# Optimization experiments

Hardware: AMD Instinct MI355X
Metric: run time of the kernel (lower is better)

The kernel has to match this reference:

```python
import jax, jax.numpy as jnp
import numpy as np

FP16_HUGE = 65504.0  # large additive mask constant (fp16-max style, as in AF2 torch ports)

B, N, T = 1, 384, 4
CQ, CT = 128, 64      # query (pair) channels, template pair channels
H = 4                 # num heads
D = CT // H           # per-head key/value dim = 16 (AF2: key_dim=value_dim=64 split over 4 heads)


def setup_inputs() -> dict:
    key = jax.random.key(0)
    ks = jax.random.split(key, 8)
    inp = {
        "query_embedding": jax.random.normal(ks[0], (B, N, N, CQ), jnp.float32),
        "template_pair_representation": jax.random.normal(ks[1], (B, T, N, N, CT), jnp.float32),
        "template_mask": jnp.ones((B, T), jnp.float32),
        # attention params (gating=False for template pointwise attention in AF2)
        "query_w": jax.random.normal(ks[2], (H, CQ, D), jnp.float32) * (CQ ** -0.5),
        "key_w": jax.random.normal(ks[3], (H, CT, D), jnp.float32) * (CT ** -0.5),
        "value_w": jax.random.normal(ks[4], (H, CT, D), jnp.float32) * (CT ** -0.5),
        "output_w": jax.random.normal(ks[5], (H, D, CQ), jnp.float32) * ((H * D) ** -0.5),
        "output_b": jnp.zeros((CQ,), jnp.float32),
    }
    return inp


def reference(query_embedding, template_pair_representation, template_mask,
              query_w, key_w, value_w, output_w, output_b):
    b, n, _, cq = query_embedding.shape
    t = template_mask.shape[-1]
    d = query_w.shape[-1]

    # [b, n*n, 1, cq]: each (i,j) pair position attends over templates
    flat_q = query_embedding.reshape(b, n * n, 1, cq)
    # [b, t, n, n, ct] -> [b, n, n, t, ct] -> [b, n*n, t, ct]
    flat_t = jnp.transpose(template_pair_representation, (0, 2, 3, 1, 4)).reshape(b, n * n, t, -1)

    # additive bias over key axis: 0 where mask=1, -FP16_HUGE where mask=0; [b,1,1,1,t]
    bias = FP16_HUGE * (template_mask[:, None, None, None, :] - 1.0)

    q = jnp.einsum('bpic,hcd->bphid', flat_q, query_w) * (d ** -0.5)  # [b,p,h,1,d]
    k = jnp.einsum('bptc,hcd->bphtd', flat_t, key_w)                  # [b,p,h,t,d]
    v = jnp.einsum('bptc,hcd->bphtd', flat_t, value_w)

    logits = jnp.einsum('bphid,bphtd->bphit', q, k) + bias            # [b,p,h,1,t]
    weights = jax.nn.softmax(logits, axis=-1)
    wv = jnp.einsum('bphit,bphtd->bphid', weights, v)                 # [b,p,h,1,d]
    out = jnp.einsum('bphid,hdc->bpic', wv, output_w) + output_b      # [b,p,1,cq]

    embedding = out.reshape(b, n, n, cq)
    tmask = (jnp.sum(template_mask.reshape(b, -1), axis=1) > 0.0).astype(embedding.dtype)
    return embedding * tmask[:, None, None, None]
```

## Files before the change

### kernel.cpp

```cpp
#include <hip/hip_runtime.h>
#include <hip/hip_bf16.h>

typedef __attribute__((ext_vector_type(8))) short bf16x8;
typedef __attribute__((ext_vector_type(4))) float f32x4;

#define NPOS 147456
#define NTILES 9216
#define TPW 2
#define WPB 4
#define NBLK (NTILES / (TPW * WPB))

__device__ inline short bfc(float f) {
  union { __hip_bfloat16 h; short s; } u;
  u.h = __float2bfloat16(f);
  return u.s;
}

__global__ __launch_bounds__(256, 2) void tpa_kernel(
    const float* __restrict__ qe, const float* __restrict__ tpr,
    const float* __restrict__ tmk_p, const float* __restrict__ wq,
    const float* __restrict__ wk, const float* __restrict__ wv,
    const float* __restrict__ wo, const float* __restrict__ ob,
    float* __restrict__ out)
{
  __shared__ unsigned short wqT[8192];
  __shared__ unsigned short woT[8192];
  __shared__ unsigned short wvbuf[WPB][1024];

  const int tid   = threadIdx.x;
  const int wid   = tid >> 6;
  const int lane  = tid & 63;
  const int row16 = lane & 15;
  const int grp   = lane >> 4;

  for (int e = tid; e < 8192; e += 256) {
    {
      int h = e >> 11, c = (e >> 4) & 127, d = e & 15;
      int col = h * 16 + d;
      wqT[(col * 128 + c) ^ ((col & 7) << 3)] = (unsigned short)bfc(wq[e] * 0.25f);
    }
    {
      int h = e >> 11, d = (e >> 7) & 15, cq = e & 127;
      int k = h * 16 + d;
      woT[(cq * 64 + k) ^ ((cq & 7) << 3)] = (unsigned short)bfc(wo[e]);
    }
  }

  bf16x8 bk[4][2], bv[4][2];
  #pragma unroll
  for (int n = 0; n < 4; ++n)
    #pragma unroll
    for (int kc = 0; kc < 2; ++kc)
      #pragma unroll
      for (int e = 0; e < 8; ++e) {
        int c = kc * 32 + grp * 8 + e;
        bk[n][kc][e] = bfc(wk[n * 1024 + c * 16 + row16]);
        bv[n][kc][e] = bfc(wv[n * 1024 + c * 16 + row16]);
      }

  const float m0 = tmk_p[0], m1 = tmk_p[1], m2 = tmk_p[2], m3 = tmk_p[3];
  const float biasv[4] = {65504.0f * (m0 - 1.0f), 65504.0f * (m1 - 1.0f),
                          65504.0f * (m2 - 1.0f), 65504.0f * (m3 - 1.0f)};
  const float tmk = (m0 + m1 + m2 + m3 > 0.0f) ? 1.0f : 0.0f;

  float obr[8];
  #pragma unroll
  for (int n8 = 0; n8 < 8; ++n8) obr[n8] = ob[n8 * 16 + row16] * tmk;

  __syncthreads();

  const int gwave = blockIdx.x * WPB + wid;

  for (int it = 0; it < TPW; ++it) {
    const int p0 = (gwave * TPW + it) * 16;

    f32x4 qv[8];
    {
      const f32x4* qbase = reinterpret_cast<const f32x4*>(qe) + (p0 + row16) * 32 + grp * 2;
      #pragma unroll
      for (int kc = 0; kc < 4; ++kc) {
        qv[kc * 2 + 0] = qbase[kc * 8 + 0];
        qv[kc * 2 + 1] = qbase[kc * 8 + 1];
      }
    }
    f32x4 tv[4][4];
    #pragma unroll
    for (int t = 0; t < 4; ++t) {
      const f32x4* tbase = reinterpret_cast<const f32x4*>(tpr) + (t * NPOS + p0 + row16) * 16 + grp * 2;
      #pragma unroll
      for (int kc = 0; kc < 2; ++kc) {
        tv[t][kc * 2 + 0] = tbase[kc * 8 + 0];
        tv[t][kc * 2 + 1] = tbase[kc * 8 + 1];
      }
    }

    bf16x8 aq[4];
    #pragma unroll
    for (int kc = 0; kc < 4; ++kc)
      #pragma unroll
      for (int e = 0; e < 8; ++e)
        aq[kc][e] = bfc(e < 4 ? qv[kc * 2 + 0][e] : qv[kc * 2 + 1][e - 4]);

    f32x4 qT[4];
    #pragma unroll
    for (int n = 0; n < 4; ++n) {
      qT[n] = (f32x4){0.f, 0.f, 0.f, 0.f};
      #pragma unroll
      for (int kc = 0; kc < 4; ++kc) {
        const bf16x8 a = *reinterpret_cast<const bf16x8*>(
            &wqT[(((n * 16 + row16) * 128) + kc * 32 + grp * 8) ^ ((row16 & 7) << 3)]);
        qT[n] = __builtin_amdgcn_mfma_f32_16x16x32_bf16(a, aq[kc], qT[n], 0, 0, 0);
      }
    }

    float ssum[4] = {0.f, 0.f, 0.f, 0.f};
    f32x4 wvT[4];
    #pragma unroll
    for (int n = 0; n < 4; ++n) wvT[n] = (f32x4){0.f, 0.f, 0.f, 0.f};

    #pragma unroll
    for (int t = 0; t < 4; ++t) {
      bf16x8 at[2];
      #pragma unroll
      for (int kc = 0; kc < 2; ++kc)
        #pragma unroll
        for (int e = 0; e < 8; ++e)
          at[kc][e] = bfc(e < 4 ? tv[t][kc * 2 + 0][e] : tv[t][kc * 2 + 1][e - 4]);

      f32x4 kT[4], vT[4];
      #pragma unroll
      for (int n = 0; n < 4; ++n) {
        kT[n] = (f32x4){0.f, 0.f, 0.f, 0.f};
        vT[n] = (f32x4){0.f, 0.f, 0.f, 0.f};
        #pragma unroll
        for (int kc = 0; kc < 2; ++kc) {
          kT[n] = __builtin_amdgcn_mfma_f32_16x16x32_bf16(bk[n][kc], at[kc], kT[n], 0, 0, 0);
          vT[n] = __builtin_amdgcn_mfma_f32_16x16x32_bf16(bv[n][kc], at[kc], vT[n], 0, 0, 0);
        }
      }
      #pragma unroll
      for (int n = 0; n < 4; ++n) {
        float lg = qT[n][0] * kT[n][0] + qT[n][1] * kT[n][1] +
                   qT[n][2] * kT[n][2] + qT[n][3] * kT[n][3];
        lg += __shfl_xor(lg, 16);
        lg += __shfl_xor(lg, 32);
        const float w = __expf(lg + biasv[t]);
        ssum[n] += w;
        #pragma unroll
        for (int r = 0; r < 4; ++r) wvT[n][r] += w * vT[n][r];
      }
    }

    #pragma unroll
    for (int n = 0; n < 4; ++n) {
      const float inv = tmk / fmaxf(ssum[n], 1e-30f);
      #pragma unroll
      for (int r = 0; r < 4; ++r) {
        const int hd = n * 16 + grp * 4 + r;
        wvbuf[wid][(row16 * 64 + hd) ^ ((row16 & 7) << 3)] =
            (unsigned short)bfc(wvT[n][r] * inv);
      }
    }
    asm volatile("s_waitcnt lgkmcnt(0)" ::: "memory");
    __builtin_amdgcn_sched_barrier(0);

    bf16x8 awv[2];
    #pragma unroll
    for (int kc = 0; kc < 2; ++kc)
      awv[kc] = *reinterpret_cast<const bf16x8*>(
          &wvbuf[wid][(row16 * 64 + kc * 32 + grp * 8) ^ ((row16 & 7) << 3)]);

    const int orow0 = p0 + grp * 4;
    #pragma unroll
    for (int n8 = 0; n8 < 8; ++n8) {
      f32x4 acc = (f32x4){0.f, 0.f, 0.f, 0.f};
      #pragma unroll
      for (int kc = 0; kc < 2; ++kc) {
        const bf16x8 b = *reinterpret_cast<const bf16x8*>(
            &woT[(((n8 * 16 + row16) * 64) + kc * 32 + grp * 8) ^ ((row16 & 7) << 3)]);
        acc = __builtin_amdgcn_mfma_f32_16x16x32_bf16(awv[kc], b, acc, 0, 0, 0);
      }
      #pragma unroll
      for (int r = 0; r < 4; ++r)
        out[(orow0 + r) * 128 + n8 * 16 + row16] = acc[r] + obr[n8];
    }
  }
}

extern "C" void kernel_launch(void* const* d_in, const int* in_sizes, int n_in,
                              void* d_out, int out_size, void* d_ws, size_t ws_size,
                              hipStream_t stream) {
  const float* qe  = (const float*)d_in[0];
  const float* tpr = (const float*)d_in[1];
  const float* tmk = (const float*)d_in[2];
  const float* wq  = (const float*)d_in[3];
  const float* wk  = (const float*)d_in[4];
  const float* wv  = (const float*)d_in[5];
  const float* wo  = (const float*)d_in[6];
  const float* ob  = (const float*)d_in[7];
  float* out = (float*)d_out;

  tpa_kernel<<<NBLK, 256, 0, stream>>>(qe, tpr, tmk, wq, wk, wv, wo, ob, out);
}
```

Before: 76.14 us.

## Pre-swizzle weights into MFMA fragments and use one-wave blocks per tile

```diff
diff --git a/kernel.cpp b/kernel.cpp
--- a/kernel.cpp
+++ b/kernel.cpp
@@ -3,187 +3,175 @@
 
 typedef __attribute__((ext_vector_type(8))) short bf16x8;
 typedef __attribute__((ext_vector_type(4))) float f32x4;
+typedef unsigned int u32;
+typedef unsigned short u16;
 
 #define NPOS 147456
 #define NTILES 9216
-#define TPW 2
-#define WPB 4
-#define NBLK (NTILES / (TPW * WPB))
 
-__device__ inline short bfc(float f) {
-  union { __hip_bfloat16 h; short s; } u;
+__device__ inline u16 bfc(float f) {
+  union { __hip_bfloat16 h; u16 s; } u;
   u.h = __float2bfloat16(f);
   return u.s;
 }
 
-__global__ __launch_bounds__(256, 2) void tpa_kernel(
+__global__ void prep_kernel(const float* __restrict__ wq, const float* __restrict__ wk,
+                            const float* __restrict__ wv, const float* __restrict__ wo,
+                            u16* __restrict__ wsf) {
+  int gid = blockIdx.x * 256 + threadIdx.x;
+  int idx, which;
+  if (gid < 8192)       { idx = gid;         which = 0; }
+  else if (gid < 12288) { idx = gid - 8192;  which = 1; }
+  else if (gid < 16384) { idx = gid - 12288; which = 2; }
+  else                  { idx = gid - 16384; which = 3; }
+  int fragid = idx >> 9, lane = (idx >> 3) & 63, e = idx & 7;
+  int l15 = lane & 15, g = lane >> 4;
+  float v;
+  if (which == 0) {
+    int n = fragid >> 2, kc = fragid & 3;
+    int c = kc * 32 + g * 8 + e;
+    v = wq[n * 2048 + c * 16 + l15] * 0.25f;
+  } else if (which == 1) {
+    int n = fragid >> 1, kc = fragid & 1;
+    int c = kc * 32 + g * 8 + e;
+    v = wk[n * 1024 + c * 16 + l15];
+  } else if (which == 2) {
+    int n = fragid >> 1, kc = fragid & 1;
+    int c = kc * 32 + g * 8 + e;
+    v = wv[n * 1024 + c * 16 + l15];
+  } else {
+    int n8 = fragid >> 1, kc = fragid & 1;
+    int hd = kc * 32 + g * 8 + e;
+    v = wo[(hd >> 4) * 2048 + (hd & 15) * 128 + n8 * 16 + l15];
+  }
+  wsf[gid] = bfc(v);
+}
+
+#define WQF(n, kc)  ((      (n) * 4 + (kc)) * 64)
+#define WKF(n, kc)  (1024 + ((n) * 2 + (kc)) * 64)
+#define WVF(n, kc)  (1536 + ((n) * 2 + (kc)) * 64)
+#define WOF(n8, kc) (2048 + ((n8) * 2 + (kc)) * 64)
+
+__global__ __launch_bounds__(64, 4) void tpa_kernel(
     const float* __restrict__ qe, const float* __restrict__ tpr,
-    const float* __restrict__ tmk_p, const float* __restrict__ wq,
-    const float* __restrict__ wk, const float* __restrict__ wv,
-    const float* __restrict__ wo, const float* __restrict__ ob,
-    float* __restrict__ out)
+    const float* __restrict__ tmk_p, const float* __restrict__ ob,
+    const u16* __restrict__ wsf, float* __restrict__ out)
 {
-  __shared__ unsigned short wqT[8192];
-  __shared__ unsigned short woT[8192];
-  __shared__ unsigned short wvbuf[WPB][1024];
-
-  const int tid   = threadIdx.x;
-  const int wid   = tid >> 6;
-  const int lane  = tid & 63;
-  const int row16 = lane & 15;
-  const int grp   = lane >> 4;
-
-  for (int e = tid; e < 8192; e += 256) {
-    {
-      int h = e >> 11, c = (e >> 4) & 127, d = e & 15;
-      int col = h * 16 + d;
-      wqT[(col * 128 + c) ^ ((col & 7) << 3)] = (unsigned short)bfc(wq[e] * 0.25f);
-    }
-    {
-      int h = e >> 11, d = (e >> 7) & 15, cq = e & 127;
-      int k = h * 16 + d;
-      woT[(cq * 64 + k) ^ ((cq & 7) << 3)] = (unsigned short)bfc(wo[e]);
-    }
-  }
-
-  bf16x8 bk[4][2], bv[4][2];
-  #pragma unroll
-  for (int n = 0; n < 4; ++n)
-    #pragma unroll
-    for (int kc = 0; kc < 2; ++kc)
-      #pragma unroll
-      for (int e = 0; e < 8; ++e) {
-        int c = kc * 32 + grp * 8 + e;
-        bk[n][kc][e] = bfc(wk[n * 1024 + c * 16 + row16]);
-        bv[n][kc][e] = bfc(wv[n * 1024 + c * 16 + row16]);
-      }
+  const int lane = threadIdx.x;
+  const int l15 = lane & 15, g = lane >> 4;
+  const int p0 = blockIdx.x * 16;
+  const bf16x8* __restrict__ wf = reinterpret_cast<const bf16x8*>(wsf);
 
   const float m0 = tmk_p[0], m1 = tmk_p[1], m2 = tmk_p[2], m3 = tmk_p[3];
   const float biasv[4] = {65504.0f * (m0 - 1.0f), 65504.0f * (m1 - 1.0f),
                           65504.0f * (m2 - 1.0f), 65504.0f * (m3 - 1.0f)};
   const float tmk = (m0 + m1 + m2 + m3 > 0.0f) ? 1.0f : 0.0f;
 
-  float obr[8];
+  const f32x4* qbase = reinterpret_cast<const f32x4*>(qe) + (p0 + l15) * 32 + g * 2;
+  f32x4 qv[8];
   #pragma unroll
-  for (int n8 = 0; n8 < 8; ++n8) obr[n8] = ob[n8 * 16 + row16] * tmk;
+  for (int kc = 0; kc < 4; ++kc) {
+    qv[kc * 2 + 0] = qbase[kc * 8 + 0];
+    qv[kc * 2 + 1] = qbase[kc * 8 + 1];
+  }
+  f32x4 tv[4][4];
+  #pragma unroll
+  for (int t = 0; t < 2; ++t) {
+    const f32x4* tbase = reinterpret_cast<const f32x4*>(tpr) +
+                         ((size_t)t * NPOS + p0 + l15) * 16 + g * 2;
+    #pragma unroll
+    for (int kc = 0; kc < 2; ++kc) {
+      tv[t][kc * 2 + 0] = tbase[kc * 8 + 0];
+      tv[t][kc * 2 + 1] = tbase[kc * 8 + 1];
+    }
+  }
 
-  __syncthreads();
+  f32x4 qT[4];
+  #pragma unroll
+  for (int n = 0; n < 4; ++n) qT[n] = (f32x4){0.f, 0.f, 0.f, 0.f};
+  #pragma unroll
+  for (int kc = 0; kc < 4; ++kc) {
+    bf16x8 aq;
+    #pragma unroll
+    for (int e = 0; e < 8; ++e)
+      aq[e] = (short)bfc(e < 4 ? qv[kc * 2 + 0][e] : qv[kc * 2 + 1][e - 4]);
+    #pragma unroll
+    for (int n = 0; n < 4; ++n)
+      qT[n] = __builtin_amdgcn_mfma_f32_16x16x32_bf16(wf[WQF(n, kc) + lane], aq, qT[n], 0, 0, 0);
+  }
 
-  const int gwave = blockIdx.x * WPB + wid;
+  float ssum[4] = {0.f, 0.f, 0.f, 0.f};
+  f32x4 wvT[4];
+  #pragma unroll
+  for (int n = 0; n < 4; ++n) wvT[n] = (f32x4){0.f, 0.f, 0.f, 0.f};
 
-  for (int it = 0; it < TPW; ++it) {
-    const int p0 = (gwave * TPW + it) * 16;
-
-    f32x4 qv[8];
-    {
-      const f32x4* qbase = reinterpret_cast<const f32x4*>(qe) + (p0 + row16) * 32 + grp * 2;
+  #pragma unroll
+  for (int t = 0; t < 4; ++t) {
+    if (t < 2) {
+      const f32x4* tbase = reinterpret_cast<const f32x4*>(tpr) +
+                           ((size_t)(t + 2) * NPOS + p0 + l15) * 16 + g * 2;
       #pragma unroll
-      for (int kc = 0; kc < 4; ++kc) {
-        qv[kc * 2 + 0] = qbase[kc * 8 + 0];
-        qv[kc * 2 + 1] = qbase[kc * 8 + 1];
+      for (int kc = 0; kc < 2; ++kc) {
+        tv[t + 2][kc * 2 + 0] = tbase[kc * 8 + 0];
+        tv[t + 2][kc * 2 + 1] = tbase[kc * 8 + 1];
       }
     }
-    f32x4 tv[4][4];
+    bf16x8 at0, at1;
     #pragma unroll
-    for (int t = 0; t < 4; ++t) {
-      const f32x4* tbase = reinterpret_cast<const f32x4*>(tpr) + (t * NPOS + p0 + row16) * 16 + grp * 2;
+    for (int e = 0; e < 8; ++e) {
+      at0[e] = (short)bfc(e < 4 ? tv[t][0][e] : tv[t][1][e - 4]);
+      at1[e] = (short)bfc(e < 4 ? tv[t][2][e] : tv[t][3][e - 4]);
+    }
+    #pragma unroll
+    for (int n = 0; n < 4; ++n) {
+      f32x4 kT = (f32x4){0.f, 0.f, 0.f, 0.f};
+      f32x4 vT = (f32x4){0.f, 0.f, 0.f, 0.f};
+      kT = __builtin_amdgcn_mfma_f32_16x16x32_bf16(wf[WKF(n, 0) + lane], at0, kT, 0, 0, 0);
+      kT = __builtin_amdgcn_mfma_f32_16x16x32_bf16(wf[WKF(n, 1) + lane], at1, kT, 0, 0, 0);
+      vT = __builtin_amdgcn_mfma_f32_16x16x32_bf16(wf[WVF(n, 0) + lane], at0, vT, 0, 0, 0);
+      vT = __builtin_amdgcn_mfma_f32_16x16x32_bf16(wf[WVF(n, 1) + lane], at1, vT, 0, 0, 0);
+      float lg = qT[n][0] * kT[0] + qT[n][1] * kT[1] + qT[n][2] * kT[2] + qT[n][3] * kT[3];
+      lg += __shfl_xor(lg, 16);
+      lg += __shfl_xor(lg, 32);
+      const float w = __expf(lg + biasv[t]);
+      ssum[n] += w;
       #pragma unroll
-      for (int kc = 0; kc < 2; ++kc) {
-        tv[t][kc * 2 + 0] = tbase[kc * 8 + 0];
-        tv[t][kc * 2 + 1] = tbase[kc * 8 + 1];
-      }
+      for (int r = 0; r < 4; ++r) wvT[n][r] += w * vT[r];
+    }
+  }
+
+  u32 pk[4][2];
+  #pragma unroll
+  for (int n = 0; n < 4; ++n) {
+    const float inv = tmk / fmaxf(ssum[n], 1e-30f);
+    pk[n][0] = (u32)bfc(wvT[n][0] * inv) | ((u32)bfc(wvT[n][1] * inv) << 16);
+    pk[n][1] = (u32)bfc(wvT[n][2] * inv) | ((u32)bfc(wvT[n][3] * inv) << 16);
+  }
+
+  union { u32 w[4]; bf16x8 v; } awv[2];
+  #pragma unroll
+  for (int kc = 0; kc < 2; ++kc)
+    #pragma unroll
+    for (int w = 0; w < 4; ++w) {
+      const int j = w & 1, hi = w >> 1;
+      const int src = l15 + 16 * ((g & 1) * 2 + hi);
+      const u32 t0 = __shfl(pk[kc * 2 + 0][j], src);
+      const u32 t1 = __shfl(pk[kc * 2 + 1][j], src);
+      awv[kc].w[w] = (g >> 1) ? t1 : t0;
     }
 
-    bf16x8 aq[4];
+  const f32x4* obase = reinterpret_cast<const f32x4*>(ob);
+  f32x4* orow = reinterpret_cast<f32x4*>(out + (size_t)(p0 + l15) * 128);
+  #pragma unroll
+  for (int n8 = 0; n8 < 8; ++n8) {
+    f32x4 acc = (f32x4){0.f, 0.f, 0.f, 0.f};
+    acc = __builtin_amdgcn_mfma_f32_16x16x32_bf16(wf[WOF(n8, 0) + lane], awv[0].v, acc, 0, 0, 0);
+    acc = __builtin_amdgcn_mfma_f32_16x16x32_bf16(wf[WOF(n8, 1) + lane], awv[1].v, acc, 0, 0, 0);
+    const f32x4 obf = obase[n8 * 4 + g];
+    f32x4 res;
     #pragma unroll
-    for (int kc = 0; kc < 4; ++kc)
-      #pragma unroll
-      for (int e = 0; e < 8; ++e)
-        aq[kc][e] = bfc(e < 4 ? qv[kc * 2 + 0][e] : qv[kc * 2 + 1][e - 4]);
-
-    f32x4 qT[4];
-    #pragma unroll
-    for (int n = 0; n < 4; ++n) {
-      qT[n] = (f32x4){0.f, 0.f, 0.f, 0.f};
-      #pragma unroll
-      for (int kc = 0; kc < 4; ++kc) {
-        const bf16x8 a = *reinterpret_cast<const bf16x8*>(
-            &wqT[(((n * 16 + row16) * 128) + kc * 32 + grp * 8) ^ ((row16 & 7) << 3)]);
-        qT[n] = __builtin_amdgcn_mfma_f32_16x16x32_bf16(a, aq[kc], qT[n], 0, 0, 0);
-      }
-    }
-
-    float ssum[4] = {0.f, 0.f, 0.f, 0.f};
-    f32x4 wvT[4];
-    #pragma unroll
-    for (int n = 0; n < 4; ++n) wvT[n] = (f32x4){0.f, 0.f, 0.f, 0.f};
-
-    #pragma unroll
-    for (int t = 0; t < 4; ++t) {
-      bf16x8 at[2];
-      #pragma unroll
-      for (int kc = 0; kc < 2; ++kc)
-        #pragma unroll
-        for (int e = 0; e < 8; ++e)
-          at[kc][e] = bfc(e < 4 ? tv[t][kc * 2 + 0][e] : tv[t][kc * 2 + 1][e - 4]);
-
-      f32x4 kT[4], vT[4];
-      #pragma unroll
-      for (int n = 0; n < 4; ++n) {
-        kT[n] = (f32x4){0.f, 0.f, 0.f, 0.f};
-        vT[n] = (f32x4){0.f, 0.f, 0.f, 0.f};
-        #pragma unroll
-        for (int kc = 0; kc < 2; ++kc) {
-          kT[n] = __builtin_amdgcn_mfma_f32_16x16x32_bf16(bk[n][kc], at[kc], kT[n], 0, 0, 0);
-          vT[n] = __builtin_amdgcn_mfma_f32_16x16x32_bf16(bv[n][kc], at[kc], vT[n], 0, 0, 0);
-        }
-      }
-      #pragma unroll
-      for (int n = 0; n < 4; ++n) {
-        float lg = qT[n][0] * kT[n][0] + qT[n][1] * kT[n][1] +
-                   qT[n][2] * kT[n][2] + qT[n][3] * kT[n][3];
-        lg += __shfl_xor(lg, 16);
-        lg += __shfl_xor(lg, 32);
-        const float w = __expf(lg + biasv[t]);
-        ssum[n] += w;
-        #pragma unroll
-        for (int r = 0; r < 4; ++r) wvT[n][r] += w * vT[n][r];
-      }
-    }
-
-    #pragma unroll
-    for (int n = 0; n < 4; ++n) {
-      const float inv = tmk / fmaxf(ssum[n], 1e-30f);
-      #pragma unroll
-      for (int r = 0; r < 4; ++r) {
-        const int hd = n * 16 + grp * 4 + r;
-        wvbuf[wid][(row16 * 64 + hd) ^ ((row16 & 7) << 3)] =
-            (unsigned short)bfc(wvT[n][r] * inv);
-      }
-    }
-    asm volatile("s_waitcnt lgkmcnt(0)" ::: "memory");
-    __builtin_amdgcn_sched_barrier(0);
-
-    bf16x8 awv[2];
-    #pragma unroll
-    for (int kc = 0; kc < 2; ++kc)
-      awv[kc] = *reinterpret_cast<const bf16x8*>(
-          &wvbuf[wid][(row16 * 64 + kc * 32 + grp * 8) ^ ((row16 & 7) << 3)]);
-
-    const int orow0 = p0 + grp * 4;
-    #pragma unroll
-    for (int n8 = 0; n8 < 8; ++n8) {
-      f32x4 acc = (f32x4){0.f, 0.f, 0.f, 0.f};
-      #pragma unroll
-      for (int kc = 0; kc < 2; ++kc) {
-        const bf16x8 b = *reinterpret_cast<const bf16x8*>(
-            &woT[(((n8 * 16 + row16) * 64) + kc * 32 + grp * 8) ^ ((row16 & 7) << 3)]);
-        acc = __builtin_amdgcn_mfma_f32_16x16x32_bf16(awv[kc], b, acc, 0, 0, 0);
-      }
-      #pragma unroll
-      for (int r = 0; r < 4; ++r)
-        out[(orow0 + r) * 128 + n8 * 16 + row16] = acc[r] + obr[n8];
-    }
+    for (int r = 0; r < 4; ++r) res[r] = acc[r] + obf[r] * tmk;
+    orow[n8 * 4 + g] = res;
   }
 }
 
@@ -199,6 +187,8 @@
   const float* wo  = (const float*)d_in[6];
   const float* ob  = (const float*)d_in[7];
   float* out = (float*)d_out;
+  u16* wsf = (u16*)d_ws;
 
-  tpa_kernel<<<NBLK, 256, 0, stream>>>(qe, tpr, tmk, wq, wk, wv, wo, ob, out);
+  prep_kernel<<<96, 256, 0, stream>>>(wq, wk, wv, wo, wsf);
+  tpa_kernel<<<NTILES, 64, 0, stream>>>(qe, tpr, tmk, ob, wsf, out);
 }
```

New measurement: 176.3 us. 132% more time.
